# Kernel optimization log

Measured on AMD Instinct MI355X. Metric: run time of the kernel, lower is better.

## Reference

```python
import jax, jax.numpy as jnp
import numpy as np

B, N, M, QD, CD, H, DH = 4, 4096, 1024, 1024, 768, 8, 64
INNER = H * DH
SCALE = DH ** -0.5


def setup_inputs() -> dict:
    key = jax.random.key(0)
    ks = jax.random.split(key, 7)
    s = 0.02  # init scale for weights
    return {
        "x": jax.random.normal(ks[0], (B, N, QD), jnp.float32),
        "context": jax.random.normal(ks[1], (B, M, CD), jnp.float32),
        "Wq": jax.random.normal(ks[2], (QD, INNER), jnp.float32) * s,   # to_q (no bias)
        "Wk": jax.random.normal(ks[3], (CD, INNER), jnp.float32) * s,   # to_k (no bias)
        "Wv": jax.random.normal(ks[4], (CD, INNER), jnp.float32) * s,   # to_v (no bias)
        "Wo": jax.random.normal(ks[5], (INNER, QD), jnp.float32) * s,   # to_out[0] weight
        "bo": jnp.zeros((QD,), jnp.float32),                             # to_out[0] bias
    }


def reference(x, context, Wq, Wk, Wv, Wo, bo):
    # Standard cross-attention path of CrossAttention.forward
    # (context given, no injected Q_c/K_s/V_s, mask=None, dropout=0 -> identity).
    b, n, _ = x.shape
    m = context.shape[1]
    # b n (h d) -> b h n d
    q = (x @ Wq).reshape(b, n, H, DH).transpose(0, 2, 1, 3)
    k = (context @ Wk).reshape(b, m, H, DH).transpose(0, 2, 1, 3)
    v = (context @ Wv).reshape(b, m, H, DH).transpose(0, 2, 1, 3)
    sim = jnp.einsum('bhid,bhjd->bhij', q, k) * SCALE  # [b,h,n,m]
    attn = jax.nn.softmax(sim, axis=-1)
    out = jnp.einsum('bhij,bhjd->bhid', attn, v)       # [b,h,n,d]
    out = out.transpose(0, 2, 1, 3).reshape(b, n, INNER)
    return out @ Wo + bo                                # [b,n,query_dim]
```

## Files before the change

### kernel.cpp

```cpp
#include <hip/hip_runtime.h>
#include <cstdint>
#include <cstddef>

typedef unsigned short u16;
typedef __attribute__((ext_vector_type(8))) __bf16 bf16x8;
typedef __attribute__((ext_vector_type(4))) float f32x4;
typedef __attribute__((ext_vector_type(4))) uint32_t u32x4;

#define B_ 4
#define N_ 4096
#define M_ 1024
#define QD_ 1024
#define CD_ 768
#define H_ 8
#define DH_ 64
#define INNER_ 512

__device__ __forceinline__ u16 f2bf(float f) {
  uint32_t u = __builtin_bit_cast(uint32_t, f);
  u += 0x7fffu + ((u >> 16) & 1u);
  return (u16)(u >> 16);
}

__device__ __forceinline__ uint32_t pk2bf(float a, float b) {
#if __has_builtin(__builtin_amdgcn_cvt_pk_bf16_f32)
  typedef __attribute__((ext_vector_type(2))) __bf16 bf16x2;
  bf16x2 r = __builtin_amdgcn_cvt_pk_bf16_f32(a, b);
  return __builtin_bit_cast(uint32_t, r);
#elif __has_builtin(__builtin_amdgcn_perm)
  uint32_t ua = __builtin_bit_cast(uint32_t, a) + 0x8000u;
  uint32_t ub = __builtin_bit_cast(uint32_t, b) + 0x8000u;
  return __builtin_amdgcn_perm(ub, ua, 0x07060302u);
#else
  return (uint32_t)f2bf(a) | ((uint32_t)f2bf(b) << 16);
#endif
}

__device__ __forceinline__ void load_lds_16B(const void* g, void* l) {
  __builtin_amdgcn_global_load_lds(
      (__attribute__((address_space(1))) void*)(void*)g,
      (__attribute__((address_space(3))) void*)l, 16, 0, 0);
}

__device__ __forceinline__ bf16x8 ldfrag(const u16* p) {
  return __builtin_bit_cast(bf16x8, *(const uint4*)p);
}

__device__ __forceinline__ uint4 pk8(float4 a, float4 b) {
  uint4 p;
  p.x = pk2bf(a.x, a.y); p.y = pk2bf(a.z, a.w);
  p.z = pk2bf(b.x, b.y); p.w = pk2bf(b.z, b.w);
  return p;
}

__global__ __launch_bounds__(256) void transpose_all(const float* __restrict__ Wq,
                                                     const float* __restrict__ Wk,
                                                     const float* __restrict__ Wv,
                                                     const float* __restrict__ Wo,
                                                     u16* __restrict__ wqT,
                                                     u16* __restrict__ wkvT,
                                                     u16* __restrict__ woT,
                                                     float cl2) {
  __shared__ float tile[32][33];
  const int bid = blockIdx.x;
  const float* in; u16* out; int R, C; float scale; int bx, by;
  if (bid < 512)       { int r = bid;        in = Wq; out = wqT;  R = 1024; C = 512;  scale = 1.f; bx = r & 15; by = r >> 4; }
  else if (bid < 896)  { int r = bid - 512;  in = Wk; out = wkvT; R = 768;  C = 512;  scale = cl2; bx = r & 15; by = r >> 4; }
  else if (bid < 1280) { int r = bid - 896;  in = Wv; out = wkvT + (size_t)512 * 768; R = 768; C = 512; scale = 1.f; bx = r & 15; by = r >> 4; }
  else                 { int r = bid - 1280; in = Wo; out = woT;  R = 512;  C = 1024; scale = 1.f; bx = r & 31; by = r >> 5; }
  int tx = threadIdx.x & 31, ty = threadIdx.x >> 5;
  int c0 = bx * 32, r0 = by * 32;
#pragma unroll
  for (int j = 0; j < 4; j++)
    tile[ty + j * 8][tx] = in[(size_t)(r0 + ty + j * 8) * C + c0 + tx];
  __syncthreads();
#pragma unroll
  for (int j = 0; j < 4; j++)
    out[(size_t)(c0 + ty + j * 8) * R + r0 + tx] = f2bf(tile[tx][ty + j * 8] * scale);
}

__global__ __launch_bounds__(256) void gemm_bt_f32a(const float* __restrict__ A,
                                                    const u16* __restrict__ Bt,
                                                    u16* __restrict__ Cout,
                                                    int M, int N, int K,
                                                    u16* __restrict__ Kc) {
  __shared__ u16 As[2][128 * 64];
  __shared__ u16 Bs[2][128 * 64];
  const int t = threadIdx.x;
  const int nwg = gridDim.x * gridDim.y;
  const int lin = blockIdx.y * gridDim.x + blockIdx.x;
  const int chunk = nwg >> 3;
  const int swz = (lin & 7) * chunk + (lin >> 3);
  const int bx = swz % gridDim.x, by = swz / gridDim.x;
  const int m0 = by * 128, n0 = bx * 128;
  const int w = t >> 6, l = t & 63, lr = l & 15, qd = l >> 4;
  const int wm = (w >> 1) * 64, wn = (w & 1) * 64;
  f32x4 acc[4][4] = {};

  const int srow[4] = { (t + 0) >> 3, (t + 256) >> 3, (t + 512) >> 3, (t + 768) >> 3 };
  const int sc8 = t & 7;
  const int lswz = sc8 ^ 0;

  {
#pragma unroll
    for (int i = 0; i < 4; i++) {
      const int row = srow[i], c8 = sc8;
      const float* s = A + (size_t)(m0 + row) * K + c8 * 8;
      float4 a0 = *(const float4*)s;
      float4 a1 = *(const float4*)(s + 4);
      *(uint4*)&As[0][row * 64 + ((c8 ^ (row & 7)) * 8)] = pk8(a0, a1);
      const int csrc = c8 ^ (row & 7);
      load_lds_16B(Bt + (size_t)(n0 + row) * K + csrc * 8, &Bs[0][(t + i * 256) * 8]);
    }
  }
  __syncthreads();

  const int NT = K >> 6;
  for (int kt = 0; kt < NT; kt++) {
    const int cur = kt & 1, nxt = cur ^ 1;
    float4 av0[4], av1[4];
    const bool pre = (kt + 1 < NT);
    if (pre) {
      const int kc = (kt + 1) * 64;
#pragma unroll
      for (int i = 0; i < 4; i++) {
        const int row = srow[i], c8 = sc8;
        const float* s = A + (size_t)(m0 + row) * K + kc + c8 * 8;
        av0[i] = *(const float4*)s;
        av1[i] = *(const float4*)(s + 4);
        const int csrc = c8 ^ (row & 7);
        load_lds_16B(Bt + (size_t)(n0 + row) * K + kc + csrc * 8, &Bs[nxt][(t + i * 256) * 8]);
      }
    }
#pragma unroll
    for (int ks = 0; ks < 2; ks++) {
      const int cs = ((ks * 4 + qd) ^ (lr & 7)) * 8;
      bf16x8 af[4], bf[4];
#pragma unroll
      for (int i = 0; i < 4; i++) af[i] = ldfrag(&As[cur][(wm + i * 16 + lr) * 64 + cs]);
#pragma unroll
      for (int j = 0; j < 4; j++) bf[j] = ldfrag(&Bs[cur][(wn + j * 16 + lr) * 64 + cs]);
#pragma unroll
      for (int mi = 0; mi < 4; mi++)
#pragma unroll
        for (int ni = 0; ni < 4; ni++)
          acc[mi][ni] = __builtin_amdgcn_mfma_f32_16x16x32_bf16(af[mi], bf[ni], acc[mi][ni], 0, 0, 0);
    }
    if (pre) {
#pragma unroll
      for (int i = 0; i < 4; i++) {
        const int row = srow[i], c8 = sc8;
        *(uint4*)&As[nxt][row * 64 + ((c8 ^ (row & 7)) * 8)] = pk8(av0[i], av1[i]);
      }
    }
    __syncthreads();
  }

  const bool kmode = (Kc != nullptr) && (n0 < 512);
  if (kmode) {
#pragma unroll
    for (int mi = 0; mi < 4; mi++)
#pragma unroll
      for (int ni = 0; ni < 4; ni++) {
        int col = n0 + wn + ni * 16 + lr;
        int h = col >> 6, c = (col >> 3) & 7, d0 = col & 7;
#pragma unroll
        for (int r = 0; r < 4; r++) {
          int row = m0 + wm + mi * 16 + qd * 4 + r;
          int b = row >> 10, m = row & 1023;
          int kt8 = m >> 7, ml = m & 127;
          size_t off = (size_t)((b << 3) + h) * 65536 + kt8 * 8192 + c * 1024 + ml * 8 + d0;
          Kc[off] = f2bf(acc[mi][ni][r]);
        }
      }
  } else {
#pragma unroll
    for (int mi = 0; mi < 4; mi++)
#pragma unroll
      for (int ni = 0; ni < 4; ni++) {
        int row = m0 + wm + mi * 16 + qd * 4;
        int col = n0 + wn + ni * 16 + lr;
#pragma unroll
        for (int r = 0; r < 4; r++)
          Cout[(size_t)(row + r) * N + col] = f2bf(acc[mi][ni][r]);
      }
  }
}

__global__ __launch_bounds__(512) void gemm256x128_bt(const u16* __restrict__ A,
                                                      const u16* __restrict__ Bt,
                                                      float* __restrict__ Cout,
                                                      int M, int N, int K,
                                                      const float* __restrict__ bias) {
  __shared__ u16 As[2][256 * 32];
  __shared__ u16 Bs[2][128 * 32];
  const int t = threadIdx.x;
  const int w = t >> 6, l = t & 63, lr = l & 15, qd = l >> 4;
  const int mw = w >> 1, nw2 = w & 1;
  const int nwg = gridDim.x * gridDim.y;
  const int lin = blockIdx.y * gridDim.x + blockIdx.x;
  const int chunk = nwg >> 3;
  const int swz = (lin & 7) * chunk + (lin >> 3);
  const int bx = swz % gridDim.x, by = swz / gridDim.x;
  const int m0 = by * 256, n0 = bx * 128;
  f32x4 acc[4][4] = {};
  const u16* ga = A + (size_t)(m0 + (t >> 2)) * K + (t & 3) * 8;
  const u16* gb = Bt + (size_t)(n0 + (t >> 2)) * K + (t & 3) * 8;

  load_lds_16B(ga, &As[0][t * 8]);
  load_lds_16B(ga + (size_t)128 * K, &As[0][(512 + t) * 8]);
  load_lds_16B(gb, &Bs[0][t * 8]);
  __syncthreads();

  const int NT = K >> 5;
  for (int kt = 0; kt < NT; kt++) {
    const int cur = kt & 1, nxt = cur ^ 1;
    if (kt + 1 < NT) {
      const int kc = (kt + 1) * 32;
      load_lds_16B(ga + kc, &As[nxt][t * 8]);
      load_lds_16B(ga + kc + (size_t)128 * K, &As[nxt][(512 + t) * 8]);
      load_lds_16B(gb + kc, &Bs[nxt][t * 8]);
    }
    bf16x8 af[4], bf[4];
#pragma unroll
    for (int i = 0; i < 4; i++) af[i] = ldfrag(&As[cur][(mw * 64 + i * 16 + lr) * 32 + qd * 8]);
#pragma unroll
    for (int j = 0; j < 4; j++) bf[j] = ldfrag(&Bs[cur][(nw2 * 64 + j * 16 + lr) * 32 + qd * 8]);
#pragma unroll
    for (int mi = 0; mi < 4; mi++)
#pragma unroll
      for (int ni = 0; ni < 4; ni++)
        acc[mi][ni] = __builtin_amdgcn_mfma_f32_16x16x32_bf16(af[mi], bf[ni], acc[mi][ni], 0, 0, 0);
    __syncthreads();
  }

#pragma unroll
  for (int mi = 0; mi < 4; mi++)
#pragma unroll
    for (int ni = 0; ni < 4; ni++) {
      int row = m0 + mw * 64 + mi * 16 + qd * 4;
      int col = n0 + nw2 * 64 + ni * 16 + lr;
#pragma unroll
      for (int r = 0; r < 4; r++)
        Cout[(size_t)(row + r) * N + col] = acc[mi][ni][r] + bias[col];
    }
}

__global__ __launch_bounds__(256) void repack_v(const u16* __restrict__ KVp,
                                                u16* __restrict__ Vtc) {
  int idx = blockIdx.x * 256 + threadIdx.x;
  int bh = idx >> 13, rest = idx & 8191;
  int kt = rest >> 10, sc = (rest >> 6) & 15, d = rest & 63;
  int b = bh >> 3, h = bh & 7;
  int g = sc >> 3, ksl = (sc >> 2) & 1, qd = sc & 3;
  ushort4 lo, hi;
  const u16* src = KVp + (size_t)(b * M_) * 1024 + 512 + h * 64 + d;
  int jb = kt * 128 + g * 64 + ksl * 16 + qd * 4;
  lo.x = src[(size_t)(jb + 0) * 1024];
  lo.y = src[(size_t)(jb + 1) * 1024];
  lo.z = src[(size_t)(jb + 2) * 1024];
  lo.w = src[(size_t)(jb + 3) * 1024];
  hi.x = src[(size_t)(jb + 32) * 1024];
  hi.y = src[(size_t)(jb + 33) * 1024];
  hi.z = src[(size_t)(jb + 34) * 1024];
  hi.w = src[(size_t)(jb + 35) * 1024];
  u16* dst = Vtc + (size_t)idx * 8;
  *(ushort4*)dst = lo;
  *(ushort4*)(dst + 4) = hi;
}

__global__ __launch_bounds__(256, 2) void attn_kernel(const u16* __restrict__ Qp,
                                                      const u16* __restrict__ Kc,
                                                      const u16* __restrict__ Vtc,
                                                      u16* __restrict__ Og) {
  __shared__ u16 Ks2[2][8192];
  __shared__ u16 Vts2[2][8192];
  const int t = threadIdx.x;
  const int w = t >> 6, l = t & 63, lr = l & 15, qd = l >> 4;
  const int nwg = gridDim.x * gridDim.y;
  const int lin = blockIdx.y * gridDim.x + blockIdx.x;
  const int chunk = nwg >> 3;
  const int swz = (lin & 7) * chunk + (lin >> 3);
  const int qt = swz % gridDim.x, bh = swz / gridDim.x;
  const int b = bh >> 3, h = bh & 7;

  const size_t qbase = ((size_t)(b * N_ + qt * 256 + w * 64)) * INNER_ + h * DH_;
  bf16x8 qf[4][2];
#pragma unroll
  for (int qt2 = 0; qt2 < 4; qt2++)
#pragma unroll
    for (int dh = 0; dh < 2; dh++)
      qf[qt2][dh] = __builtin_bit_cast(bf16x8,
          *(const uint4*)(Qp + qbase + (size_t)(qt2 * 16 + lr) * INNER_ + dh * 32 + qd * 8));

  f32x4 oacc[4][4] = {};
  f32x4 lacc[4] = {};
  const u16* ksrc0 = Kc + (size_t)bh * 65536;
  const u16* vsrc0 = Vtc + (size_t)bh * 65536;

  u32x4 onesw;
  onesw[0] = 0x3F803F80u; onesw[1] = 0x3F803F80u; onesw[2] = 0x3F803F80u; onesw[3] = 0x3F803F80u;
  const bf16x8 onesf = __builtin_bit_cast(bf16x8, onesw);

#pragma unroll
  for (int i = 0; i < 4; i++) load_lds_16B(ksrc0 + (i * 256 + t) * 8, &Ks2[0][(i * 256 + t) * 8]);
#pragma unroll
  for (int i = 0; i < 4; i++) load_lds_16B(vsrc0 + (i * 256 + t) * 8, &Vts2[0][(i * 256 + t) * 8]);
  __syncthreads();

  for (int kt = 0; kt < 8; kt++) {
    const int cur = kt & 1, nxt = cur ^ 1;
    if (kt < 7) {
      const u16* kn = ksrc0 + (kt + 1) * 8192;
      const u16* vn = vsrc0 + (kt + 1) * 8192;
#pragma unroll
      for (int i = 0; i < 4; i++) load_lds_16B(kn + (i * 256 + t) * 8, &Ks2[nxt][(i * 256 + t) * 8]);
#pragma unroll
      for (int i = 0; i < 4; i++) load_lds_16B(vn + (i * 256 + t) * 8, &Vts2[nxt][(i * 256 + t) * 8]);
    }
    const u16* Ksc = Ks2[cur];
    const u16* Vsc = Vts2[cur];

#pragma unroll
    for (int g = 0; g < 2; g++) {
      f32x4 sacc[4][4] = {};
#pragma unroll
      for (int jt = 0; jt < 4; jt++)
#pragma unroll
        for (int dh = 0; dh < 2; dh++) {
          bf16x8 kf = ldfrag(&Ksc[(dh * 4 + qd) * 1024 + (g * 64 + jt * 16 + lr) * 8]);
#pragma unroll
          for (int qt2 = 0; qt2 < 4; qt2++)
            sacc[jt][qt2] = __builtin_amdgcn_mfma_f32_16x16x32_bf16(kf, qf[qt2][dh], sacc[jt][qt2], 0, 0, 0);
        }
#pragma unroll
      for (int jt = 0; jt < 4; jt++)
#pragma unroll
        for (int qt2 = 0; qt2 < 4; qt2++)
#pragma unroll
          for (int r = 0; r < 4; r++)
            sacc[jt][qt2][r] = __builtin_amdgcn_exp2f(sacc[jt][qt2][r]);
      u32x4 pk[4][2];
#pragma unroll
      for (int qt2 = 0; qt2 < 4; qt2++)
#pragma unroll
        for (int ksl = 0; ksl < 2; ksl++)
#pragma unroll
          for (int v = 0; v < 4; v++) {
            int jt = (v >> 1) * 2 + ksl, r = (v & 1) * 2;
            pk[qt2][ksl][v] = pk2bf(sacc[jt][qt2][r], sacc[jt][qt2][r + 1]);
          }
#pragma unroll
      for (int ksl = 0; ksl < 2; ksl++) {
#pragma unroll
        for (int dt = 0; dt < 4; dt++) {
          bf16x8 vf = ldfrag(&Vsc[(g * 8 + ksl * 4 + qd) * 512 + (dt * 16 + lr) * 8]);
#pragma unroll
          for (int qt2 = 0; qt2 < 4; qt2++)
            oacc[qt2][dt] = __builtin_amdgcn_mfma_f32_16x16x32_bf16(
                vf, __builtin_bit_cast(bf16x8, pk[qt2][ksl]), oacc[qt2][dt], 0, 0, 0);
        }
#pragma unroll
        for (int qt2 = 0; qt2 < 4; qt2++)
          lacc[qt2] = __builtin_amdgcn_mfma_f32_16x16x32_bf16(
              onesf, __builtin_bit_cast(bf16x8, pk[qt2][ksl]), lacc[qt2], 0, 0, 0);
      }
    }
    __syncthreads();
  }

#pragma unroll
  for (int qt2 = 0; qt2 < 4; qt2++) {
    float inv = 1.f / lacc[qt2][0];
    int q = qt * 256 + w * 64 + qt2 * 16 + lr;
    size_t base = ((size_t)(b * N_ + q)) * INNER_ + h * DH_ + qd * 4;
#pragma unroll
    for (int dt = 0; dt < 4; dt++) {
      uint2 o;
      o.x = pk2bf(oacc[qt2][dt][0] * inv, oacc[qt2][dt][1] * inv);
      o.y = pk2bf(oacc[qt2][dt][2] * inv, oacc[qt2][dt][3] * inv);
      *(uint2*)(Og + base + dt * 16) = o;
    }
  }
}

extern "C" void kernel_launch(void* const* d_in, const int* in_sizes, int n_in,
                              void* d_out, int out_size, void* d_ws, size_t ws_size,
                              hipStream_t stream) {
  const float* x   = (const float*)d_in[0];
  const float* ctx = (const float*)d_in[1];
  const float* Wq  = (const float*)d_in[2];
  const float* Wk  = (const float*)d_in[3];
  const float* Wv  = (const float*)d_in[4];
  const float* Wo  = (const float*)d_in[5];
  const float* bo  = (const float*)d_in[6];
  float* out = (float*)d_out;

  const float cl2 = 0.18033688011112042f;

  u16* wqT  = (u16*)d_ws;
  u16* wkvT = wqT  + (size_t)512 * 1024;
  u16* woT  = wkvT + (size_t)1024 * 768;
  u16* Qp   = woT  + (size_t)1024 * 512;
  u16* Kc   = Qp   + (size_t)16384 * 512;
  u16* Vtc  = Kc   + (size_t)32 * 65536;
  u16* Og   = Vtc  + (size_t)32 * 65536;
  u16* KVp  = Og;

  transpose_all<<<1792, 256, 0, stream>>>(Wq, Wk, Wv, Wo, wqT, wkvT, woT, cl2);

  gemm_bt_f32a<<<dim3(4, 128), 256, 0, stream>>>(x, wqT, Qp, 16384, 512, 1024, nullptr);
  gemm_bt_f32a<<<dim3(8, 32), 256, 0, stream>>>(ctx, wkvT, KVp, 4096, 1024, 768, Kc);
  repack_v<<<1024, 256, 0, stream>>>(KVp, Vtc);

  attn_kernel<<<dim3(16, 32), 256, 0, stream>>>(Qp, Kc, Vtc, Og);

  gemm256x128_bt<<<dim3(8, 64), 512, 0, stream>>>(Og, woT, out, 16384, 1024, 512, bo);
}
```

Baseline: 251.4 us.

## Fuse Q and KV projection GEMMs into one launch and write V pre-packed

Merges the Q projection and the K/V projection into a single grid of 768 blocks, choosing the operands by block index. The V half now writes straight into the packed layout the attention kernel reads, so the separate repack_v kernel and the KVp scratch round trip are gone. This saves two launches, one intermediate write and read of V, and fills the machine better by running both GEMMs together. In exchange, the V epilogue does scattered 2-byte stores, and blocks with different K lengths share one grid, which may leave the tail of the launch unbalanced.

```diff
diff --git a/kernel.cpp b/kernel.cpp
--- a/kernel.cpp
+++ b/kernel.cpp
@@ -79,19 +79,23 @@
     out[(size_t)(c0 + ty + j * 8) * R + r0 + tx] = f2bf(tile[tx][ty + j * 8] * scale);
 }
 
-__global__ __launch_bounds__(256) void gemm_bt_f32a(const float* __restrict__ A,
-                                                    const u16* __restrict__ Bt,
-                                                    u16* __restrict__ Cout,
-                                                    int M, int N, int K,
-                                                    u16* __restrict__ Kc) {
+__global__ __launch_bounds__(256) void gemm_fused_proj(const float* __restrict__ x,
+                                                       const float* __restrict__ ctx,
+                                                       const u16* __restrict__ wqT,
+                                                       const u16* __restrict__ wkvT,
+                                                       u16* __restrict__ Qp,
+                                                       u16* __restrict__ Kc,
+                                                       u16* __restrict__ Vtc) {
   __shared__ u16 As[2][128 * 64];
   __shared__ u16 Bs[2][128 * 64];
   const int t = threadIdx.x;
-  const int nwg = gridDim.x * gridDim.y;
-  const int lin = blockIdx.y * gridDim.x + blockIdx.x;
+  const bool isQ = (blockIdx.x < 512);
+  const float* A; const u16* Bt; int K, lin, nwg, gx;
+  if (isQ) { A = x;   Bt = wqT;  K = 1024; lin = blockIdx.x;       nwg = 512; gx = 4; }
+  else     { A = ctx; Bt = wkvT; K = 768;  lin = blockIdx.x - 512; nwg = 256; gx = 8; }
   const int chunk = nwg >> 3;
   const int swz = (lin & 7) * chunk + (lin >> 3);
-  const int bx = swz % gridDim.x, by = swz / gridDim.x;
+  const int bx = swz % gx, by = swz / gx;
   const int m0 = by * 128, n0 = bx * 128;
   const int w = t >> 6, l = t & 63, lr = l & 15, qd = l >> 4;
   const int wm = (w >> 1) * 64, wn = (w & 1) * 64;
@@ -99,7 +103,6 @@
 
   const int srow[4] = { (t + 0) >> 3, (t + 256) >> 3, (t + 512) >> 3, (t + 768) >> 3 };
   const int sc8 = t & 7;
-  const int lswz = sc8 ^ 0;
 
   {
 #pragma unroll
@@ -156,8 +159,18 @@
     __syncthreads();
   }
 
-  const bool kmode = (Kc != nullptr) && (n0 < 512);
-  if (kmode) {
+  if (isQ) {
+#pragma unroll
+    for (int mi = 0; mi < 4; mi++)
+#pragma unroll
+      for (int ni = 0; ni < 4; ni++) {
+        int row = m0 + wm + mi * 16 + qd * 4;
+        int col = n0 + wn + ni * 16 + lr;
+#pragma unroll
+        for (int r = 0; r < 4; r++)
+          Qp[(size_t)(row + r) * 512 + col] = f2bf(acc[mi][ni][r]);
+      }
+  } else if (n0 < 512) {
 #pragma unroll
     for (int mi = 0; mi < 4; mi++)
 #pragma unroll
@@ -178,11 +191,21 @@
     for (int mi = 0; mi < 4; mi++)
 #pragma unroll
       for (int ni = 0; ni < 4; ni++) {
-        int row = m0 + wm + mi * 16 + qd * 4;
         int col = n0 + wn + ni * 16 + lr;
-#pragma unroll
-        for (int r = 0; r < 4; r++)
-          Cout[(size_t)(row + r) * N + col] = f2bf(acc[mi][ni][r]);
+        int cv = col - 512;
+        int h = cv >> 6, d = cv & 63;
+#pragma unroll
+        for (int r = 0; r < 4; r++) {
+          int row = m0 + wm + mi * 16 + qd * 4 + r;
+          int b = row >> 10, m = row & 1023;
+          int kt8 = m >> 7, mrem = m & 127;
+          int g = mrem >> 6, s = mrem & 63;
+          int hi = s >> 5, ksl = (s >> 4) & 1, qdv = (s >> 2) & 3, rr = s & 3;
+          int e = rr + (hi << 2);
+          int sc = g * 8 + ksl * 4 + qdv;
+          size_t off = (size_t)((b << 3) + h) * 65536 + kt8 * 8192 + sc * 512 + d * 8 + e;
+          Vtc[off] = f2bf(acc[mi][ni][r]);
+        }
       }
   }
 }
@@ -246,29 +269,6 @@
     }
 }
 
-__global__ __launch_bounds__(256) void repack_v(const u16* __restrict__ KVp,
-                                                u16* __restrict__ Vtc) {
-  int idx = blockIdx.x * 256 + threadIdx.x;
-  int bh = idx >> 13, rest = idx & 8191;
-  int kt = rest >> 10, sc = (rest >> 6) & 15, d = rest & 63;
-  int b = bh >> 3, h = bh & 7;
-  int g = sc >> 3, ksl = (sc >> 2) & 1, qd = sc & 3;
-  ushort4 lo, hi;
-  const u16* src = KVp + (size_t)(b * M_) * 1024 + 512 + h * 64 + d;
-  int jb = kt * 128 + g * 64 + ksl * 16 + qd * 4;
-  lo.x = src[(size_t)(jb + 0) * 1024];
-  lo.y = src[(size_t)(jb + 1) * 1024];
-  lo.z = src[(size_t)(jb + 2) * 1024];
-  lo.w = src[(size_t)(jb + 3) * 1024];
-  hi.x = src[(size_t)(jb + 32) * 1024];
-  hi.y = src[(size_t)(jb + 33) * 1024];
-  hi.z = src[(size_t)(jb + 34) * 1024];
-  hi.w = src[(size_t)(jb + 35) * 1024];
-  u16* dst = Vtc + (size_t)idx * 8;
-  *(ushort4*)dst = lo;
-  *(ushort4*)(dst + 4) = hi;
-}
-
 __global__ __launch_bounds__(256, 2) void attn_kernel(const u16* __restrict__ Qp,
                                                       const u16* __restrict__ Kc,
                                                       const u16* __restrict__ Vtc,
@@ -405,13 +405,10 @@
   u16* Kc   = Qp   + (size_t)16384 * 512;
   u16* Vtc  = Kc   + (size_t)32 * 65536;
   u16* Og   = Vtc  + (size_t)32 * 65536;
-  u16* KVp  = Og;
 
   transpose_all<<<1792, 256, 0, stream>>>(Wq, Wk, Wv, Wo, wqT, wkvT, woT, cl2);
 
-  gemm_bt_f32a<<<dim3(4, 128), 256, 0, stream>>>(x, wqT, Qp, 16384, 512, 1024, nullptr);
-  gemm_bt_f32a<<<dim3(8, 32), 256, 0, stream>>>(ctx, wkvT, KVp, 4096, 1024, 768, Kc);
-  repack_v<<<1024, 256, 0, stream>>>(KVp, Vtc);
+  gemm_fused_proj<<<768, 256, 0, stream>>>(x, ctx, wqT, wkvT, Qp, Kc, Vtc);
 
   attn_kernel<<<dim3(16, 32), 256, 0, stream>>>(Qp, Kc, Vtc, Og);
 
```

After: 245.3 us. 2.4% less time.
